# Optimization experiments

Hardware: AMD Instinct MI355X
Metric: run time of the kernel (lower is better)

## Reference

```python
import jax, jax.numpy as jnp
import numpy as np

B, N, M, C, H, NNZ = 64, 2048, 2048, 64, 128, 32768


def setup_inputs() -> dict:
    key = jax.random.key(0)
    ks = jax.random.split(key, 7)
    x = jax.random.normal(ks[0], (B * N, H), dtype=jnp.float32)
    batch = jnp.repeat(jnp.arange(B, dtype=jnp.int32), N)  # sorted graph ids
    d_rows = jax.random.randint(ks[1], (B, NNZ), 0, M, dtype=jnp.int32)
    d_cols = jax.random.randint(ks[2], (B, NNZ), 0, N, dtype=jnp.int32)
    d_vals = jax.random.normal(ks[3], (B, NNZ), dtype=jnp.float32) * (1.0 / np.sqrt(16.0))
    d_index = jax.random.randint(ks[4], (B, M), 0, C, dtype=jnp.int32)
    w_scale = 1.0 / np.sqrt(3 * H)
    Wq = jax.random.normal(ks[5], (3 * H, H), dtype=jnp.float32) * w_scale
    Wk = jax.random.normal(ks[6], (3 * H, H), dtype=jnp.float32) * w_scale
    Wv = jax.random.normal(jax.random.fold_in(key, 7), (3 * H, H), dtype=jnp.float32) * w_scale
    return {"x": x, "batch": batch, "batch_size": B, "d_rows": d_rows,
            "d_cols": d_cols, "d_vals": d_vals, "d_index": d_index,
            "Wq": Wq, "Wk": Wk, "Wv": Wv}


def _per_graph(xg, rows, cols, vals, idx, Wq, Wk, Wv):
    # spmm: coefs[r] = sum_e vals[e] * xg[cols[e]] for rows[e] == r  -> [M, H]
    coefs = jax.ops.segment_sum(vals[:, None] * xg[cols], rows, num_segments=M)
    # three segment poolings over cluster index -> each [C, H]
    s = jax.ops.segment_sum(coefs, idx, num_segments=C)
    cnt = jax.ops.segment_sum(jnp.ones((M,), coefs.dtype), idx, num_segments=C)
    mean = s / jnp.maximum(cnt, 1.0)[:, None]
    mx = jax.ops.segment_max(coefs, idx, num_segments=C)
    x_dec = jnp.concatenate([mean, mx, s], axis=1)  # [C, 3H]
    # small self-attention over clusters (linear layers without bias)
    Q = x_dec @ Wq
    K = x_dec @ Wk
    V = x_dec @ Wv
    dist = jax.nn.softmax((Q @ K.T) * (1.0 / np.sqrt(H)), axis=-1)
    return (dist @ V).reshape(-1)  # [C*H]


def reference(x, batch, batch_size, d_rows, d_cols, d_vals, d_index, Wq, Wk, Wv):
    # nodes are sorted by graph with equal graph size N, so x[batch==i] == xb[i]
    xb = x.reshape(batch_size, N, H)
    out = jax.vmap(_per_graph, in_axes=(0, 0, 0, 0, 0, None, None, None))(
        xb, d_rows, d_cols, d_vals, d_index, Wq, Wk, Wv)
    return out  # [B, C*H] == torch.vstack of per-graph flattened attentions
```

## Files before the change

### kernel.cpp

```cpp
#include <hip/hip_runtime.h>
#include <hip/hip_fp16.h>

#define BG 64
#define NN 2048
#define MM 2048
#define CC 64
#define HH 128
#define NNZE 32768
#define TH 384

typedef float f4v __attribute__((ext_vector_type(4)));

__global__ __launch_bounds__(256) void cvt_x_kernel(const float* __restrict__ x,
                                                    uint* __restrict__ xh) {
    int bid = blockIdx.x;
    int j = bid >> 3;
    int g = ((bid & 7) << 3) + (j >> 7);
    int chunk = j & 127;
    int tid = g * 32768 + chunk * 256 + threadIdx.x;
    const f4v* x4 = (const f4v*)x;
    f4v a = __builtin_nontemporal_load(&x4[2 * tid]);
    f4v b = __builtin_nontemporal_load(&x4[2 * tid + 1]);
    __half2 h0 = __float22half2_rn(make_float2(a.x, a.y));
    __half2 h1 = __float22half2_rn(make_float2(a.z, a.w));
    __half2 h2 = __float22half2_rn(make_float2(b.x, b.y));
    __half2 h3 = __float22half2_rn(make_float2(b.z, b.w));
    uint4 o;
    o.x = *(uint*)&h0;
    o.y = *(uint*)&h1;
    o.z = *(uint*)&h2;
    o.w = *(uint*)&h3;
    ((uint4*)xh)[tid] = o;
}

__global__ __launch_bounds__(1024) void prep_count_kernel(const int* __restrict__ d_rows,
                                                          const int* __restrict__ d_index,
                                                          int* __restrict__ cnt_blk,
                                                          int* __restrict__ cnt_clu_blk) {
    __shared__ int cnt_row_s[MM];
    __shared__ int cnt_clu_s[CC];
    int gb = blockIdx.x;
    int g = gb >> 2, b = gb & 3;
    int t = threadIdx.x;
    cnt_row_s[t] = 0;
    cnt_row_s[t + 1024] = 0;
    if (t < CC) cnt_clu_s[t] = 0;
    __syncthreads();
    const int* rows_g = d_rows + ((size_t)g << 15) + (b << 13);
#pragma unroll
    for (int it = 0; it < 8; it++) atomicAdd(&cnt_row_s[rows_g[it * 1024 + t]], 1);
    if (t < 512) atomicAdd(&cnt_clu_s[d_index[(g << 11) + (b << 9) + t]], 1);
    __syncthreads();
    int* cb = cnt_blk + (size_t)gb * MM;
    cb[t] = cnt_row_s[t];
    cb[t + 1024] = cnt_row_s[t + 1024];
    if (t < CC) cnt_clu_blk[gb * CC + t] = cnt_clu_s[t];
}

__global__ __launch_bounds__(1024) void prep_scan_kernel(const int* __restrict__ d_index,
                                                         const int* __restrict__ cnt_blk,
                                                         const int* __restrict__ cnt_clu_blk,
                                                         int* __restrict__ cnt_clu_g,
                                                         int* __restrict__ off_clu_g,
                                                         int* __restrict__ row_edge_off_g,
                                                         int* __restrict__ off_row_blk,
                                                         int* __restrict__ end_pos) {
    __shared__ int cnt_clu_s[CC], off_clu_s[CC], fill_clu_s[CC];
    __shared__ int rlist_s[MM];
    __shared__ int rowtot_s[MM];
    __shared__ int blk1_s[MM], blk2_s[MM], blk3_s[MM];
    __shared__ int off_row_s[MM];
    __shared__ int wsum[16];
    int g = blockIdx.x, t = threadIdx.x;
    int lane = t & 63, w = t >> 6;

    const int* cb = cnt_blk + ((size_t)g << 2) * MM;
    for (int r = t; r < MM; r += 1024) {
        int c0 = cb[r], c1 = cb[MM + r], c2 = cb[2 * MM + r], c3 = cb[3 * MM + r];
        blk1_s[r] = c0;
        blk2_s[r] = c0 + c1;
        blk3_s[r] = c0 + c1 + c2;
        rowtot_s[r] = c0 + c1 + c2 + c3;
    }
    if (t < CC) {
        const int* ccb = cnt_clu_blk + (g << 2) * CC;
        int v = ccb[t] + ccb[CC + t] + ccb[2 * CC + t] + ccb[3 * CC + t];
        cnt_clu_s[t] = v;
        fill_clu_s[t] = 0;
        int incl = v;
#pragma unroll
        for (int d = 1; d < 64; d <<= 1) {
            int u = __shfl_up(incl, d);
            if (t >= d) incl += u;
        }
        off_clu_s[t] = incl - v;
        cnt_clu_g[(g << 6) + t] = v;
        off_clu_g[(g << 6) + t] = incl - v;
    }
    int idx0 = d_index[(g << 11) + t];
    int idx1 = d_index[(g << 11) + t + 1024];
    __syncthreads();

    {
        int s0 = atomicAdd(&fill_clu_s[idx0], 1);
        rlist_s[off_clu_s[idx0] + s0] = t;
        int s1 = atomicAdd(&fill_clu_s[idx1], 1);
        rlist_s[off_clu_s[idx1] + s1] = t + 1024;
    }
    __syncthreads();

    int r0 = rlist_s[2 * t], r1 = rlist_s[2 * t + 1];
    int c0 = rowtot_s[r0], c1 = rowtot_s[r1];
    int s = c0 + c1;
    int incl = s;
#pragma unroll
    for (int d = 1; d < 64; d <<= 1) {
        int u = __shfl_up(incl, d);
        if (lane >= d) incl += u;
    }
    if (lane == 63) wsum[w] = incl;
    __syncthreads();
    if (t < 16) {
        int v = wsum[t], iv = v;
#pragma unroll
        for (int d = 1; d < 16; d <<= 1) {
            int u = __shfl_up(iv, d);
            if (t >= d) iv += u;
        }
        wsum[t] = iv - v;
    }
    __syncthreads();
    {
        int base = wsum[w] + incl - s;
        int* reo = row_edge_off_g + g * (MM + 1);
        reo[2 * t] = base;
        reo[2 * t + 1] = base + c0;
        off_row_s[r0] = base;
        off_row_s[r1] = base + c0;
        if (t == 0) reo[MM] = NNZE;
    }
    __syncthreads();

    int* ob = off_row_blk + ((size_t)g << 2) * MM;
    int* epp = end_pos + (size_t)g * MM;
    for (int r = t; r < MM; r += 1024) {
        int orr = off_row_s[r];
        ob[r] = orr;
        ob[MM + r] = orr + blk1_s[r];
        ob[2 * MM + r] = orr + blk2_s[r];
        ob[3 * MM + r] = orr + blk3_s[r];
        epp[r] = orr + rowtot_s[r];
    }
}

__global__ __launch_bounds__(1024) void prep_bin_kernel(const int* __restrict__ d_rows,
                                                        const int* __restrict__ d_cols,
                                                        const float* __restrict__ d_vals,
                                                        const int* __restrict__ off_row_blk,
                                                        const int* __restrict__ end_pos,
                                                        int2* __restrict__ epack) {
    __shared__ int off_s[MM];
    __shared__ int end_s[MM];
    __shared__ int fill_s[MM];
    int gb = blockIdx.x;
    int g = gb >> 2, b = gb & 3;
    int t = threadIdx.x;
    const int* ob = off_row_blk + (size_t)gb * MM;
    const int* epp = end_pos + (size_t)g * MM;
    off_s[t] = ob[t];
    off_s[t + 1024] = ob[t + 1024];
    end_s[t] = epp[t];
    end_s[t + 1024] = epp[t + 1024];
    fill_s[t] = 0;
    fill_s[t + 1024] = 0;
    __syncthreads();
    const int* rows_g = d_rows + ((size_t)g << 15) + (b << 13);
    const int* cols_g = d_cols + ((size_t)g << 15) + (b << 13);
    const float* vals_g = d_vals + ((size_t)g << 15) + (b << 13);
    int2* epg = epack + ((size_t)g << 15);
#pragma unroll
    for (int it = 0; it < 8; it++) {
        int e = it * 1024 + t;
        int r = rows_g[e];
        int slot = atomicAdd(&fill_s[r], 1);
        int pos = off_s[r] + slot;
        int flag = (pos == end_s[r] - 1) ? (int)0x80000000 : 0;
        epg[pos] = make_int2(cols_g[e] | flag, __float_as_int(vals_g[e]));
    }
}

__global__ __launch_bounds__(64) void spmm_pool_kernel(const uint* __restrict__ xh,
                                                       const int* __restrict__ cnt_clu,
                                                       const int* __restrict__ off_clu,
                                                       const int* __restrict__ row_edge_off,
                                                       const int2* __restrict__ epack,
                                                       float* __restrict__ xdec) {
    int bid = blockIdx.x;
    int l = bid >> 3;
    int g = ((bid & 7) << 3) + (l >> 6);
    int c = l & 63;
    int h = threadIdx.x;
    int gc = (g << 6) + c;
    int rcnt = cnt_clu[gc];
    int j0 = off_clu[gc];
    const int* reo = row_edge_off + g * (MM + 1) + j0;
    int ebase = reo[0];
    int etot = reo[rcnt] - ebase;
    const long long* ep = (const long long*)(epack + ((size_t)g << 15)) + ebase;
    const uint* xg = xh + ((size_t)g << 17);
    float2 coef = make_float2(0.f, 0.f), sum = make_float2(0.f, 0.f);
    float2 mx = make_float2(-__builtin_inff(), -__builtin_inff());
    int e = 0;
    for (; e + 16 <= etot; e += 16) {
        long long q[16];
#pragma unroll
        for (int k = 0; k < 16; k++) q[k] = __builtin_nontemporal_load(&ep[e + k]);
        uint xv[16];
#pragma unroll
        for (int k = 0; k < 16; k++)
            xv[k] = xg[(((uint)(int)q[k] & 0x7FFFFFFFu) << 6) + h];
#pragma unroll
        for (int k = 0; k < 16; k++) {
            float v = __int_as_float((int)(q[k] >> 32));
            float2 f = __half22float2(*(__half2*)&xv[k]);
            coef.x = fmaf(v, f.x, coef.x);
            coef.y = fmaf(v, f.y, coef.y);
            if ((int)q[k] < 0) {
                sum.x += coef.x; sum.y += coef.y;
                mx.x = fmaxf(mx.x, coef.x); mx.y = fmaxf(mx.y, coef.y);
                coef.x = 0.f; coef.y = 0.f;
            }
        }
    }
    for (; e < etot; e++) {
        long long q = ep[e];
        uint xv = xg[(((uint)(int)q & 0x7FFFFFFFu) << 6) + h];
        float v = __int_as_float((int)(q >> 32));
        float2 f = __half22float2(*(__half2*)&xv);
        coef.x = fmaf(v, f.x, coef.x);
        coef.y = fmaf(v, f.y, coef.y);
        if ((int)q < 0) {
            sum.x += coef.x; sum.y += coef.y;
            mx.x = fmaxf(mx.x, coef.x); mx.y = fmaxf(mx.y, coef.y);
            coef.x = 0.f; coef.y = 0.f;
        }
    }
    int az = 0;
    for (int j = h; j < rcnt; j += 64) az |= (reo[j + 1] == reo[j]);
    if (__ballot(az) != 0ULL) {
        mx.x = fmaxf(mx.x, 0.f);
        mx.y = fmaxf(mx.y, 0.f);
    }
    float inv = 1.f / (float)(rcnt > 0 ? rcnt : 1);
    float* xd = xdec + (size_t)gc * TH;
    *(float2*)&xd[2 * h] = make_float2(sum.x * inv, sum.y * inv);
    *(float2*)&xd[HH + 2 * h] = mx;
    *(float2*)&xd[2 * HH + 2 * h] = sum;
}

__global__ __launch_bounds__(256) void qkv_kernel(const float* __restrict__ xdec,
                                                  const float* __restrict__ Wq,
                                                  const float* __restrict__ Wk,
                                                  const float* __restrict__ Wv,
                                                  float* __restrict__ QKV) {
    __shared__ float As[16][68];
    __shared__ float Bs[16][64];
    int bx = blockIdx.x, by = blockIdx.y;
    int t = threadIdx.x;
    int tx = t & 15, ty = t >> 4;
    const float* W = (by < 2) ? Wq : (by < 4) ? Wk : Wv;
    int cbase = (by & 1) * 64;
    int r0 = bx * 64;
    float acc[4][4] = {};
    int lrow = t >> 2, lk4 = (t & 3) * 4;
    for (int k0 = 0; k0 < TH; k0 += 16) {
        float4 av = *(const float4*)&xdec[(size_t)(r0 + lrow) * TH + k0 + lk4];
        As[lk4][lrow] = av.x;
        As[lk4 + 1][lrow] = av.y;
        As[lk4 + 2][lrow] = av.z;
        As[lk4 + 3][lrow] = av.w;
        *(float4*)&Bs[ty][tx * 4] = *(const float4*)&W[(size_t)(k0 + ty) * HH + cbase + tx * 4];
        __syncthreads();
#pragma unroll
        for (int k = 0; k < 16; k++) {
            float4 a = *(float4*)&As[k][ty * 4];
            float4 b = *(float4*)&Bs[k][tx * 4];
            float ar[4] = {a.x, a.y, a.z, a.w};
            float br[4] = {b.x, b.y, b.z, b.w};
#pragma unroll
            for (int i = 0; i < 4; i++)
#pragma unroll
                for (int j = 0; j < 4; j++) acc[i][j] = fmaf(ar[i], br[j], acc[i][j]);
        }
        __syncthreads();
    }
#pragma unroll
    for (int i = 0; i < 4; i++) {
        *(float4*)&QKV[(size_t)(r0 + ty * 4 + i) * TH + by * 64 + tx * 4] =
            make_float4(acc[i][0], acc[i][1], acc[i][2], acc[i][3]);
    }
}

__global__ __launch_bounds__(256) void attn_kernel(const float* __restrict__ QKV,
                                                   float* __restrict__ out) {
    __shared__ float Qs[16][132];
    __shared__ float sc[16][68];
    int g = blockIdx.x;
    int q0 = blockIdx.y * 16;
    int t = threadIdx.x;
    const float* base = QKV + (size_t)(g * CC) * TH;
    for (int u = t; u < 512; u += 256) {
        int i = u >> 5, cc = u & 31;
        *(float4*)&Qs[i][cc * 4] = *(const float4*)&base[(size_t)(q0 + i) * TH + cc * 4];
    }
    __syncthreads();
    {
        int j = t & 63, iq = t >> 6;
        float a0 = 0, a1 = 0, a2 = 0, a3 = 0;
        const float* Krow = base + (size_t)j * TH + HH;
#pragma unroll 4
        for (int cc = 0; cc < 32; cc++) {
            float4 kv = *(const float4*)&Krow[cc * 4];
            float4 q0v = *(float4*)&Qs[iq][cc * 4];
            float4 q1v = *(float4*)&Qs[4 + iq][cc * 4];
            float4 q2v = *(float4*)&Qs[8 + iq][cc * 4];
            float4 q3v = *(float4*)&Qs[12 + iq][cc * 4];
            a0 += kv.x * q0v.x + kv.y * q0v.y + kv.z * q0v.z + kv.w * q0v.w;
            a1 += kv.x * q1v.x + kv.y * q1v.y + kv.z * q1v.z + kv.w * q1v.w;
            a2 += kv.x * q2v.x + kv.y * q2v.y + kv.z * q2v.z + kv.w * q2v.w;
            a3 += kv.x * q3v.x + kv.y * q3v.y + kv.z * q3v.z + kv.w * q3v.w;
        }
        const float scale = 0.08838834764831845f;
        sc[iq][j] = a0 * scale;
        sc[4 + iq][j] = a1 * scale;
        sc[8 + iq][j] = a2 * scale;
        sc[12 + iq][j] = a3 * scale;
    }
    __syncthreads();
    {
        int i = t >> 4, l = t & 15;
        float4 sv = *(float4*)&sc[i][l * 4];
        float m = fmaxf(fmaxf(sv.x, sv.y), fmaxf(sv.z, sv.w));
#pragma unroll
        for (int d = 1; d < 16; d <<= 1) m = fmaxf(m, __shfl_xor(m, d));
        float4 p;
        p.x = __expf(sv.x - m);
        p.y = __expf(sv.y - m);
        p.z = __expf(sv.z - m);
        p.w = __expf(sv.w - m);
        float s = p.x + p.y + p.z + p.w;
#pragma unroll
        for (int d = 1; d < 16; d <<= 1) s += __shfl_xor(s, d);
        float inv = 1.0f / s;
        p.x *= inv; p.y *= inv; p.z *= inv; p.w *= inv;
        *(float4*)&sc[i][l * 4] = p;
    }
    __syncthreads();
    {
        int i = t >> 4, hq = t & 15;
        const float* Vbase = base + 2 * HH;
        float acc[8] = {};
        for (int j = 0; j < 64; j++) {
            float d = sc[i][j];
            float4 v0 = *(const float4*)&Vbase[(size_t)j * TH + hq * 8];
            float4 v1 = *(const float4*)&Vbase[(size_t)j * TH + hq * 8 + 4];
            acc[0] = fmaf(d, v0.x, acc[0]);
            acc[1] = fmaf(d, v0.y, acc[1]);
            acc[2] = fmaf(d, v0.z, acc[2]);
            acc[3] = fmaf(d, v0.w, acc[3]);
            acc[4] = fmaf(d, v1.x, acc[4]);
            acc[5] = fmaf(d, v1.y, acc[5]);
            acc[6] = fmaf(d, v1.z, acc[6]);
            acc[7] = fmaf(d, v1.w, acc[7]);
        }
        float* op = out + (size_t)g * (CC * HH) + (size_t)(q0 + i) * HH + hq * 8;
        *(float4*)&op[0] = make_float4(acc[0], acc[1], acc[2], acc[3]);
        *(float4*)&op[4] = make_float4(acc[4], acc[5], acc[6], acc[7]);
    }
}

extern "C" void kernel_launch(void* const* d_in, const int* in_sizes, int n_in,
                              void* d_out, int out_size, void* d_ws, size_t ws_size,
                              hipStream_t stream) {
    const float* x = (const float*)d_in[0];
    const int* d_rows = (const int*)d_in[3];
    const int* d_cols = (const int*)d_in[4];
    const float* d_vals = (const float*)d_in[5];
    const int* d_index = (const int*)d_in[6];
    const float* Wq = (const float*)d_in[7];
    const float* Wk = (const float*)d_in[8];
    const float* Wv = (const float*)d_in[9];
    float* out = (float*)d_out;

    char* ws = (char*)d_ws;
    size_t o = 0;
    uint* xh = (uint*)(ws + o); o += (size_t)BG * NN * (HH / 2) * 4;
    int2* epack = (int2*)(ws + o); o += (size_t)BG * NNZE * 8;
    int* cnt_blk = (int*)(ws + o); o += (size_t)BG * 4 * MM * 4;
    int* off_row_blk = (int*)(ws + o); o += (size_t)BG * 4 * MM * 4;
    int* end_pos = (int*)(ws + o); o += (size_t)BG * MM * 4;
    int* cnt_clu_blk = (int*)(ws + o); o += (size_t)BG * 4 * CC * 4;
    int* row_edge_off = (int*)(ws + o); o += (size_t)BG * (MM + 1) * 4;
    int* cnt_clu = (int*)(ws + o); o += (size_t)BG * CC * 4;
    int* off_clu = (int*)(ws + o); o += (size_t)BG * CC * 4;
    float* xdec = (float*)(ws + o); o += (size_t)BG * CC * TH * 4;
    float* QKV = (float*)(ws + o); o += (size_t)BG * CC * TH * 4;

    prep_count_kernel<<<BG * 4, 1024, 0, stream>>>(d_rows, d_index, cnt_blk, cnt_clu_blk);
    prep_scan_kernel<<<BG, 1024, 0, stream>>>(d_index, cnt_blk, cnt_clu_blk,
                                              cnt_clu, off_clu, row_edge_off,
                                              off_row_blk, end_pos);
    prep_bin_kernel<<<BG * 4, 1024, 0, stream>>>(d_rows, d_cols, d_vals,
                                                 off_row_blk, end_pos, epack);
    cvt_x_kernel<<<BG * NN * HH / 8 / 256, 256, 0, stream>>>(x, xh);
    spmm_pool_kernel<<<BG * CC, 64, 0, stream>>>(xh, cnt_clu, off_clu, row_edge_off,
                                                 epack, xdec);
    qkv_kernel<<<dim3(64, 6), 256, 0, stream>>>(xdec, Wq, Wk, Wv, QKV);
    attn_kernel<<<dim3(BG, 4), 256, 0, stream>>>(QKV, out);
}
```

Baseline: 261.7 us.

## Split wavefront halves across edge pairs with 8-byte gathers in spmm_pool

The spmm pooling kernel now has each 64-lane wavefront handle two edges at a time. Each half-wave gathers one column row of x with 8-byte (4 half) loads instead of 4-byte loads. Partial row coefficients are combined across the halves with a shuffle when a row ends. Occupancy is hinted with launch_bounds(64,4), and the unroll depth grows to 32 edges. This halves the number of gather instructions per edge and widens each memory access, at the cost of extra shuffles and branching at row boundaries.

```diff
diff --git a/kernel.cpp b/kernel.cpp
--- a/kernel.cpp
+++ b/kernel.cpp
@@ -189,17 +189,19 @@
     }
 }
 
-__global__ __launch_bounds__(64) void spmm_pool_kernel(const uint* __restrict__ xh,
-                                                       const int* __restrict__ cnt_clu,
-                                                       const int* __restrict__ off_clu,
-                                                       const int* __restrict__ row_edge_off,
-                                                       const int2* __restrict__ epack,
-                                                       float* __restrict__ xdec) {
+__global__ __launch_bounds__(64, 4) void spmm_pool_kernel(const uint* __restrict__ xh,
+                                                          const int* __restrict__ cnt_clu,
+                                                          const int* __restrict__ off_clu,
+                                                          const int* __restrict__ row_edge_off,
+                                                          const int2* __restrict__ epack,
+                                                          float* __restrict__ xdec) {
     int bid = blockIdx.x;
     int l = bid >> 3;
     int g = ((bid & 7) << 3) + (l >> 6);
     int c = l & 63;
-    int h = threadIdx.x;
+    int t = threadIdx.x;
+    int f = t & 31;
+    int hi = t & 32;
     int gc = (g << 6) + c;
     int rcnt = cnt_clu[gc];
     int j0 = off_clu[gc];
@@ -207,55 +209,113 @@
     int ebase = reo[0];
     int etot = reo[rcnt] - ebase;
     const long long* ep = (const long long*)(epack + ((size_t)g << 15)) + ebase;
-    const uint* xg = xh + ((size_t)g << 17);
-    float2 coef = make_float2(0.f, 0.f), sum = make_float2(0.f, 0.f);
-    float2 mx = make_float2(-__builtin_inff(), -__builtin_inff());
+    const uint2* xg2 = (const uint2*)(xh + ((size_t)g << 17));
+    float4 coef = make_float4(0.f, 0.f, 0.f, 0.f);
+    float4 sum = make_float4(0.f, 0.f, 0.f, 0.f);
+    float4 mx = make_float4(-__builtin_inff(), -__builtin_inff(),
+                            -__builtin_inff(), -__builtin_inff());
+
+#define ACCUM(XV, VV)                                      \
+    do {                                                   \
+        float2 _f0 = __half22float2(*(__half2*)&(XV).x);   \
+        float2 _f1 = __half22float2(*(__half2*)&(XV).y);   \
+        float _vv = (VV);                                  \
+        coef.x = fmaf(_vv, _f0.x, coef.x);                 \
+        coef.y = fmaf(_vv, _f0.y, coef.y);                 \
+        coef.z = fmaf(_vv, _f1.x, coef.z);                 \
+        coef.w = fmaf(_vv, _f1.y, coef.w);                 \
+    } while (0)
+
+#define FLUSH                                              \
+    do {                                                   \
+        float _tx = coef.x + __shfl_xor(coef.x, 32);       \
+        float _ty = coef.y + __shfl_xor(coef.y, 32);       \
+        float _tz = coef.z + __shfl_xor(coef.z, 32);       \
+        float _tw = coef.w + __shfl_xor(coef.w, 32);       \
+        sum.x += _tx; sum.y += _ty; sum.z += _tz; sum.w += _tw; \
+        mx.x = fmaxf(mx.x, _tx); mx.y = fmaxf(mx.y, _ty);  \
+        mx.z = fmaxf(mx.z, _tz); mx.w = fmaxf(mx.w, _tw);  \
+        coef.x = 0.f; coef.y = 0.f; coef.z = 0.f; coef.w = 0.f; \
+    } while (0)
+
+#define PAIR_STEP(Q0, Q1, XV)                              \
+    do {                                                   \
+        float _v0 = __int_as_float((int)((Q0) >> 32));     \
+        float _v1 = __int_as_float((int)((Q1) >> 32));     \
+        bool _fl0 = (int)(Q0) < 0, _fl1 = (int)(Q1) < 0;   \
+        if (!_fl0 && !_fl1) {                              \
+            ACCUM(XV, hi ? _v1 : _v0);                     \
+        } else {                                           \
+            ACCUM(XV, hi ? 0.f : _v0);                     \
+            if (_fl0) FLUSH;                               \
+            ACCUM(XV, hi ? _v1 : 0.f);                     \
+            if (_fl1) FLUSH;                               \
+        }                                                  \
+    } while (0)
+
     int e = 0;
-    for (; e + 16 <= etot; e += 16) {
-        long long q[16];
-#pragma unroll
-        for (int k = 0; k < 16; k++) q[k] = __builtin_nontemporal_load(&ep[e + k]);
-        uint xv[16];
-#pragma unroll
-        for (int k = 0; k < 16; k++)
-            xv[k] = xg[(((uint)(int)q[k] & 0x7FFFFFFFu) << 6) + h];
-#pragma unroll
-        for (int k = 0; k < 16; k++) {
-            float v = __int_as_float((int)(q[k] >> 32));
-            float2 f = __half22float2(*(__half2*)&xv[k]);
-            coef.x = fmaf(v, f.x, coef.x);
-            coef.y = fmaf(v, f.y, coef.y);
-            if ((int)q[k] < 0) {
-                sum.x += coef.x; sum.y += coef.y;
-                mx.x = fmaxf(mx.x, coef.x); mx.y = fmaxf(mx.y, coef.y);
-                coef.x = 0.f; coef.y = 0.f;
-            }
-        }
-    }
-    for (; e < etot; e++) {
-        long long q = ep[e];
-        uint xv = xg[(((uint)(int)q & 0x7FFFFFFFu) << 6) + h];
-        float v = __int_as_float((int)(q >> 32));
-        float2 f = __half22float2(*(__half2*)&xv);
-        coef.x = fmaf(v, f.x, coef.x);
-        coef.y = fmaf(v, f.y, coef.y);
-        if ((int)q < 0) {
-            sum.x += coef.x; sum.y += coef.y;
-            mx.x = fmaxf(mx.x, coef.x); mx.y = fmaxf(mx.y, coef.y);
-            coef.x = 0.f; coef.y = 0.f;
-        }
-    }
+    for (; e + 32 <= etot; e += 32) {
+        long long q[32];
+#pragma unroll
+        for (int k = 0; k < 32; k++) q[k] = __builtin_nontemporal_load(&ep[e + k]);
+        uint2 xv[16];
+#pragma unroll
+        for (int p = 0; p < 16; p++) {
+            int c0 = (int)q[2 * p] & 0x7FFFFFFF;
+            int c1 = (int)q[2 * p + 1] & 0x7FFFFFFF;
+            xv[p] = xg2[((uint)(hi ? c1 : c0) << 5) + f];
+        }
+#pragma unroll
+        for (int p = 0; p < 16; p++) PAIR_STEP(q[2 * p], q[2 * p + 1], xv[p]);
+    }
+    for (; e + 8 <= etot; e += 8) {
+        long long q[8];
+#pragma unroll
+        for (int k = 0; k < 8; k++) q[k] = __builtin_nontemporal_load(&ep[e + k]);
+        uint2 xv[4];
+#pragma unroll
+        for (int p = 0; p < 4; p++) {
+            int c0 = (int)q[2 * p] & 0x7FFFFFFF;
+            int c1 = (int)q[2 * p + 1] & 0x7FFFFFFF;
+            xv[p] = xg2[((uint)(hi ? c1 : c0) << 5) + f];
+        }
+#pragma unroll
+        for (int p = 0; p < 4; p++) PAIR_STEP(q[2 * p], q[2 * p + 1], xv[p]);
+    }
+    for (; e + 2 <= etot; e += 2) {
+        long long q0 = __builtin_nontemporal_load(&ep[e]);
+        long long q1 = __builtin_nontemporal_load(&ep[e + 1]);
+        int c0 = (int)q0 & 0x7FFFFFFF;
+        int c1 = (int)q1 & 0x7FFFFFFF;
+        uint2 xv = xg2[((uint)(hi ? c1 : c0) << 5) + f];
+        PAIR_STEP(q0, q1, xv);
+    }
+    if (e < etot) {
+        long long q0 = __builtin_nontemporal_load(&ep[e]);
+        int c0 = (int)q0 & 0x7FFFFFFF;
+        uint2 xv = xg2[((uint)c0 << 5) + f];
+        ACCUM(xv, hi ? 0.f : __int_as_float((int)(q0 >> 32)));
+        if ((int)q0 < 0) FLUSH;
+    }
+
     int az = 0;
-    for (int j = h; j < rcnt; j += 64) az |= (reo[j + 1] == reo[j]);
+    for (int j = t; j < rcnt; j += 64) az |= (reo[j + 1] == reo[j]);
     if (__ballot(az) != 0ULL) {
         mx.x = fmaxf(mx.x, 0.f);
         mx.y = fmaxf(mx.y, 0.f);
+        mx.z = fmaxf(mx.z, 0.f);
+        mx.w = fmaxf(mx.w, 0.f);
     }
     float inv = 1.f / (float)(rcnt > 0 ? rcnt : 1);
-    float* xd = xdec + (size_t)gc * TH;
-    *(float2*)&xd[2 * h] = make_float2(sum.x * inv, sum.y * inv);
-    *(float2*)&xd[HH + 2 * h] = mx;
-    *(float2*)&xd[2 * HH + 2 * h] = sum;
+    if (t < 32) {
+        float* xd = xdec + (size_t)gc * TH;
+        *(float4*)&xd[4 * f] = make_float4(sum.x * inv, sum.y * inv, sum.z * inv, sum.w * inv);
+        *(float4*)&xd[HH + 4 * f] = mx;
+        *(float4*)&xd[2 * HH + 4 * f] = sum;
+    }
+#undef ACCUM
+#undef FLUSH
+#undef PAIR_STEP
 }
 
 __global__ __launch_bounds__(256) void qkv_kernel(const float* __restrict__ xdec,
```

Result: slower. 270.9 us (+3.5%).

## Double-buffer SpMM gathers into LDS via async global_load_lds with prefetched edge batches

Applied to the files above, without the earlier changes.

The SpMM pooling loop now handles edges in batches of 32. For each batch, the gathered half-precision rows of x are staged into a double-buffered LDS tile with 16-byte global_load_lds, and edge metadata is prefetched two batches ahead. Each lane now loads one packed edge and the per-edge column/value are broadcast with readlane, instead of every lane loading every edge. This is meant to overlap the gather latency of the next batch with compute on the current one, in exchange for 16KB of LDS per 64-thread block (lower occupancy) and explicit vmcnt waits.

```diff
diff --git a/kernel.cpp b/kernel.cpp
--- a/kernel.cpp
+++ b/kernel.cpp
@@ -10,6 +10,11 @@
 #define TH 384
 
 typedef float f4v __attribute__((ext_vector_type(4)));
+
+#define GLOAD_LDS16(SRC, DST)                                             \
+    __builtin_amdgcn_global_load_lds(                                     \
+        (const __attribute__((address_space(1))) uint*)(SRC),             \
+        (__attribute__((address_space(3))) uint*)(DST), 16, 0, 0)
 
 __global__ __launch_bounds__(256) void cvt_x_kernel(const float* __restrict__ x,
                                                     uint* __restrict__ xh) {
@@ -195,11 +200,14 @@
                                                        const int* __restrict__ row_edge_off,
                                                        const int2* __restrict__ epack,
                                                        float* __restrict__ xdec) {
+    __shared__ uint sbuf[2][2048];
     int bid = blockIdx.x;
     int l = bid >> 3;
     int g = ((bid & 7) << 3) + (l >> 6);
     int c = l & 63;
     int h = threadIdx.x;
+    int sub = h >> 4;
+    int part = h & 15;
     int gc = (g << 6) + c;
     int rcnt = cnt_clu[gc];
     int j0 = off_clu[gc];
@@ -210,41 +218,84 @@
     const uint* xg = xh + ((size_t)g << 17);
     float2 coef = make_float2(0.f, 0.f), sum = make_float2(0.f, 0.f);
     float2 mx = make_float2(-__builtin_inff(), -__builtin_inff());
-    int e = 0;
-    for (; e + 16 <= etot; e += 16) {
-        long long q[16];
-#pragma unroll
-        for (int k = 0; k < 16; k++) q[k] = __builtin_nontemporal_load(&ep[e + k]);
-        uint xv[16];
-#pragma unroll
-        for (int k = 0; k < 16; k++)
-            xv[k] = xg[(((uint)(int)q[k] & 0x7FFFFFFFu) << 6) + h];
-#pragma unroll
-        for (int k = 0; k < 16; k++) {
-            float v = __int_as_float((int)(q[k] >> 32));
-            float2 f = __half22float2(*(__half2*)&xv[k]);
-            coef.x = fmaf(v, f.x, coef.x);
-            coef.y = fmaf(v, f.y, coef.y);
-            if ((int)q[k] < 0) {
-                sum.x += coef.x; sum.y += coef.y;
-                mx.x = fmaxf(mx.x, coef.x); mx.y = fmaxf(mx.y, coef.y);
-                coef.x = 0.f; coef.y = 0.f;
+
+#define SPMM_FLUSH                                         \
+    do {                                                   \
+        sum.x += coef.x; sum.y += coef.y;                  \
+        mx.x = fmaxf(mx.x, coef.x);                        \
+        mx.y = fmaxf(mx.y, coef.y);                        \
+        coef.x = 0.f; coef.y = 0.f;                        \
+    } while (0)
+
+    int nb = etot >> 5;
+    long long qC = 0, qA = 0, qB = 0;
+    int colA[8], colB[8];
+    int cur = 0;
+
+    if (nb > 0) {
+        qC = ep[h >> 1];
+        int col0[8];
+#pragma unroll
+        for (int i = 0; i < 8; i++)
+            col0[i] = ((const int*)(ep + 4 * i + sub))[0] & 0x7FFFFFFF;
+        asm volatile("s_waitcnt vmcnt(0)" ::: "memory");
+#pragma unroll
+        for (int i = 0; i < 8; i++)
+            GLOAD_LDS16(xg + ((uint)col0[i] << 6) + (part << 2), &sbuf[0][i << 8]);
+        if (nb > 1) {
+            const long long* ep1 = ep + 32;
+            qA = ep1[h >> 1];
+#pragma unroll
+            for (int i = 0; i < 8; i++)
+                colA[i] = ((const int*)(ep1 + 4 * i + sub))[0] & 0x7FFFFFFF;
+        }
+    }
+    for (int b = 0; b < nb; b++) {
+        asm volatile("s_waitcnt vmcnt(0)" ::: "memory");
+        if (b + 1 < nb) {
+#pragma unroll
+            for (int i = 0; i < 8; i++)
+                GLOAD_LDS16(xg + ((uint)colA[i] << 6) + (part << 2),
+                            &sbuf[cur ^ 1][i << 8]);
+        }
+        if (b + 2 < nb) {
+            const long long* epn = ep + ((b + 2) << 5);
+            qB = epn[h >> 1];
+#pragma unroll
+            for (int i = 0; i < 8; i++)
+                colB[i] = ((const int*)(epn + 4 * i + sub))[0] & 0x7FFFFFFF;
+        }
+        {
+            int qlo = (int)qC, qhi = (int)(qC >> 32);
+            const uint* sb = &sbuf[cur][0];
+#pragma unroll
+            for (int k = 0; k < 32; k++) {
+                uint xv = sb[(k << 6) + h];
+                int ql = __builtin_amdgcn_readlane(qlo, 2 * k);
+                int qh = __builtin_amdgcn_readlane(qhi, 2 * k);
+                float v = __int_as_float(qh);
+                float2 f = __half22float2(*(__half2*)&xv);
+                coef.x = fmaf(v, f.x, coef.x);
+                coef.y = fmaf(v, f.y, coef.y);
+                if (ql < 0) SPMM_FLUSH;
             }
         }
-    }
-    for (; e < etot; e++) {
+        qC = qA;
+        qA = qB;
+#pragma unroll
+        for (int i = 0; i < 8; i++) colA[i] = colB[i];
+        cur ^= 1;
+    }
+    for (int e = nb << 5; e < etot; e++) {
         long long q = ep[e];
         uint xv = xg[(((uint)(int)q & 0x7FFFFFFFu) << 6) + h];
         float v = __int_as_float((int)(q >> 32));
         float2 f = __half22float2(*(__half2*)&xv);
         coef.x = fmaf(v, f.x, coef.x);
         coef.y = fmaf(v, f.y, coef.y);
-        if ((int)q < 0) {
-            sum.x += coef.x; sum.y += coef.y;
-            mx.x = fmaxf(mx.x, coef.x); mx.y = fmaxf(mx.y, coef.y);
-            coef.x = 0.f; coef.y = 0.f;
-        }
-    }
+        if ((int)q < 0) SPMM_FLUSH;
+    }
+
     int az = 0;
     for (int j = h; j < rcnt; j += 64) az |= (reo[j + 1] == reo[j]);
     if (__ballot(az) != 0ULL) {
@@ -256,6 +307,7 @@
     *(float2*)&xd[2 * h] = make_float2(sum.x * inv, sum.y * inv);
     *(float2*)&xd[HH + 2 * h] = mx;
     *(float2*)&xd[2 * HH + 2 * h] = sum;
+#undef SPMM_FLUSH
 }
 
 __global__ __launch_bounds__(256) void qkv_kernel(const float* __restrict__ xdec,
```

New measurement: 286.7 us. 9.5% more time.

## Use split-bf16 MFMA for QKV projection and fuse x conversion into prep

Applied to the files above, without the earlier changes.

The QKV projection moves from an FP32 SIMT GEMM to bf16 MFMA instructions, using a hi/lo split (three products per tile) to keep close to FP32 accuracy. The spmm kernel now writes the pooled features as hi/lo bf16 pairs, and the weights are split and transposed inside the prep count kernel. The separate x-to-half conversion kernel is folded into prep_count, removing one launch. The cost is three MFMAs per tile plus the extra split work, and prep_count now does more memory traffic per block.

```diff
diff --git a/kernel.cpp b/kernel.cpp
--- a/kernel.cpp
+++ b/kernel.cpp
@@ -10,33 +10,30 @@
 #define TH 384
 
 typedef float f4v __attribute__((ext_vector_type(4)));
-
-__global__ __launch_bounds__(256) void cvt_x_kernel(const float* __restrict__ x,
-                                                    uint* __restrict__ xh) {
-    int bid = blockIdx.x;
-    int j = bid >> 3;
-    int g = ((bid & 7) << 3) + (j >> 7);
-    int chunk = j & 127;
-    int tid = g * 32768 + chunk * 256 + threadIdx.x;
-    const f4v* x4 = (const f4v*)x;
-    f4v a = __builtin_nontemporal_load(&x4[2 * tid]);
-    f4v b = __builtin_nontemporal_load(&x4[2 * tid + 1]);
-    __half2 h0 = __float22half2_rn(make_float2(a.x, a.y));
-    __half2 h1 = __float22half2_rn(make_float2(a.z, a.w));
-    __half2 h2 = __float22half2_rn(make_float2(b.x, b.y));
-    __half2 h3 = __float22half2_rn(make_float2(b.z, b.w));
-    uint4 o;
-    o.x = *(uint*)&h0;
-    o.y = *(uint*)&h1;
-    o.z = *(uint*)&h2;
-    o.w = *(uint*)&h3;
-    ((uint4*)xh)[tid] = o;
+typedef __attribute__((ext_vector_type(8))) short bf16x8;
+typedef __attribute__((ext_vector_type(4))) float f32x4;
+typedef unsigned short u16;
+
+static __device__ __forceinline__ u16 bf16rne(float f) {
+    uint u = __float_as_uint(f);
+    uint r = u + 0x7FFFu + ((u >> 16) & 1u);
+    return (u16)(r >> 16);
+}
+static __device__ __forceinline__ float bf16tof(u16 h) {
+    return __uint_as_float(((uint)h) << 16);
 }
 
 __global__ __launch_bounds__(1024) void prep_count_kernel(const int* __restrict__ d_rows,
                                                           const int* __restrict__ d_index,
+                                                          const float* __restrict__ x,
+                                                          const float* __restrict__ Wq,
+                                                          const float* __restrict__ Wk,
+                                                          const float* __restrict__ Wv,
                                                           int* __restrict__ cnt_blk,
-                                                          int* __restrict__ cnt_clu_blk) {
+                                                          int* __restrict__ cnt_clu_blk,
+                                                          uint* __restrict__ xh,
+                                                          u16* __restrict__ WhT,
+                                                          u16* __restrict__ WlT) {
     __shared__ int cnt_row_s[MM];
     __shared__ int cnt_clu_s[CC];
     int gb = blockIdx.x;
@@ -50,6 +47,39 @@
 #pragma unroll
     for (int it = 0; it < 8; it++) atomicAdd(&cnt_row_s[rows_g[it * 1024 + t]], 1);
     if (t < 512) atomicAdd(&cnt_clu_s[d_index[(g << 11) + (b << 9) + t]], 1);
+
+    {
+        const f4v* x4 = (const f4v*)x;
+        uint4* xh4 = (uint4*)xh;
+#pragma unroll
+        for (int it = 0; it < 8; it++) {
+            int tidg = (gb << 13) + it * 1024 + t;
+            f4v a = __builtin_nontemporal_load(&x4[2 * tidg]);
+            f4v bb = __builtin_nontemporal_load(&x4[2 * tidg + 1]);
+            __half2 h0 = __float22half2_rn(make_float2(a.x, a.y));
+            __half2 h1 = __float22half2_rn(make_float2(a.z, a.w));
+            __half2 h2 = __float22half2_rn(make_float2(bb.x, bb.y));
+            __half2 h3 = __float22half2_rn(make_float2(bb.z, bb.w));
+            uint4 o;
+            o.x = *(uint*)&h0;
+            o.y = *(uint*)&h1;
+            o.z = *(uint*)&h2;
+            o.w = *(uint*)&h3;
+            xh4[tidg] = o;
+        }
+    }
+    if (gb < 144) {
+        int id = (gb << 10) + t;
+        int w = id / 49152;
+        int r = id - w * 49152;
+        const float* Ws = (w == 0) ? Wq : (w == 1) ? Wk : Wv;
+        float v = Ws[r];
+        int k = r >> 7, n = r & 127;
+        u16 hi = bf16rne(v);
+        u16 lo = bf16rne(v - bf16tof(hi));
+        WhT[w * 49152 + n * 384 + k] = hi;
+        WlT[w * 49152 + n * 384 + k] = lo;
+    }
     __syncthreads();
     int* cb = cnt_blk + (size_t)gb * MM;
     cb[t] = cnt_row_s[t];
@@ -194,7 +224,8 @@
                                                        const int* __restrict__ off_clu,
                                                        const int* __restrict__ row_edge_off,
                                                        const int2* __restrict__ epack,
-                                                       float* __restrict__ xdec) {
+                                                       u16* __restrict__ xdh,
+                                                       u16* __restrict__ xdl) {
     int bid = blockIdx.x;
     int l = bid >> 3;
     int g = ((bid & 7) << 3) + (l >> 6);
@@ -252,53 +283,91 @@
         mx.y = fmaxf(mx.y, 0.f);
     }
     float inv = 1.f / (float)(rcnt > 0 ? rcnt : 1);
-    float* xd = xdec + (size_t)gc * TH;
-    *(float2*)&xd[2 * h] = make_float2(sum.x * inv, sum.y * inv);
-    *(float2*)&xd[HH + 2 * h] = mx;
-    *(float2*)&xd[2 * HH + 2 * h] = sum;
-}
-
-__global__ __launch_bounds__(256) void qkv_kernel(const float* __restrict__ xdec,
-                                                  const float* __restrict__ Wq,
-                                                  const float* __restrict__ Wk,
-                                                  const float* __restrict__ Wv,
+    uint* oh = (uint*)xdh + (size_t)gc * 192 + h;
+    uint* ol = (uint*)xdl + (size_t)gc * 192 + h;
+    float me0 = sum.x * inv, me1 = sum.y * inv;
+    u16 a0 = bf16rne(me0), a1 = bf16rne(me1);
+    oh[0] = (uint)a0 | ((uint)a1 << 16);
+    ol[0] = (uint)bf16rne(me0 - bf16tof(a0)) | ((uint)bf16rne(me1 - bf16tof(a1)) << 16);
+    u16 b0 = bf16rne(mx.x), b1 = bf16rne(mx.y);
+    oh[64] = (uint)b0 | ((uint)b1 << 16);
+    ol[64] = (uint)bf16rne(mx.x - bf16tof(b0)) | ((uint)bf16rne(mx.y - bf16tof(b1)) << 16);
+    u16 c0 = bf16rne(sum.x), c1 = bf16rne(sum.y);
+    oh[128] = (uint)c0 | ((uint)c1 << 16);
+    ol[128] = (uint)bf16rne(sum.x - bf16tof(c0)) | ((uint)bf16rne(sum.y - bf16tof(c1)) << 16);
+}
+
+__global__ __launch_bounds__(256) void qkv_kernel(const u16* __restrict__ xdh,
+                                                  const u16* __restrict__ xdl,
+                                                  const u16* __restrict__ WhT,
+                                                  const u16* __restrict__ WlT,
                                                   float* __restrict__ QKV) {
-    __shared__ float As[16][68];
-    __shared__ float Bs[16][64];
+    __shared__ u16 Ah[64][40], Al[64][40], Bh[64][40], Bl[64][40];
     int bx = blockIdx.x, by = blockIdx.y;
     int t = threadIdx.x;
-    int tx = t & 15, ty = t >> 4;
-    const float* W = (by < 2) ? Wq : (by < 4) ? Wk : Wv;
-    int cbase = (by & 1) * 64;
-    int r0 = bx * 64;
-    float acc[4][4] = {};
-    int lrow = t >> 2, lk4 = (t & 3) * 4;
-    for (int k0 = 0; k0 < TH; k0 += 16) {
-        float4 av = *(const float4*)&xdec[(size_t)(r0 + lrow) * TH + k0 + lk4];
-        As[lk4][lrow] = av.x;
-        As[lk4 + 1][lrow] = av.y;
-        As[lk4 + 2][lrow] = av.z;
-        As[lk4 + 3][lrow] = av.w;
-        *(float4*)&Bs[ty][tx * 4] = *(const float4*)&W[(size_t)(k0 + ty) * HH + cbase + tx * 4];
+    int w = by >> 1;
+    int cb = (by & 1) << 6;
+    int r0 = bx << 6;
+    const u16* wh = WhT + w * 49152;
+    const u16* wl = WlT + w * 49152;
+    int lane = t & 63, wv = t >> 6;
+    int wm = wv >> 1, wn = wv & 1;
+    int srow = t >> 2, sks = (t & 3) << 3;
+    int fr = lane & 15, fk = (lane >> 4) << 3;
+    f32x4 acc[2][2];
+#pragma unroll
+    for (int i = 0; i < 2; i++)
+#pragma unroll
+        for (int j = 0; j < 2; j++)
+#pragma unroll
+            for (int r = 0; r < 4; r++) acc[i][j][r] = 0.f;
+    for (int ks = 0; ks < 12; ks++) {
+        int k0 = ks << 5;
+        bf16x8 sa_h = *(const bf16x8*)&xdh[(size_t)(r0 + srow) * 384 + k0 + sks];
+        bf16x8 sa_l = *(const bf16x8*)&xdl[(size_t)(r0 + srow) * 384 + k0 + sks];
+        bf16x8 sb_h = *(const bf16x8*)&wh[(size_t)(cb + srow) * 384 + k0 + sks];
+        bf16x8 sb_l = *(const bf16x8*)&wl[(size_t)(cb + srow) * 384 + k0 + sks];
+        if (ks) __syncthreads();
+        *(bf16x8*)&Ah[srow][sks] = sa_h;
+        *(bf16x8*)&Al[srow][sks] = sa_l;
+        *(bf16x8*)&Bh[srow][sks] = sb_h;
+        *(bf16x8*)&Bl[srow][sks] = sb_l;
         __syncthreads();
-#pragma unroll
-        for (int k = 0; k < 16; k++) {
-            float4 a = *(float4*)&As[k][ty * 4];
-            float4 b = *(float4*)&Bs[k][tx * 4];
-            float ar[4] = {a.x, a.y, a.z, a.w};
-            float br[4] = {b.x, b.y, b.z, b.w};
-#pragma unroll
-            for (int i = 0; i < 4; i++)
-#pragma unroll
-                for (int j = 0; j < 4; j++) acc[i][j] = fmaf(ar[i], br[j], acc[i][j]);
-        }
-        __syncthreads();
-    }
-#pragma unroll
-    for (int i = 0; i < 4; i++) {
-        *(float4*)&QKV[(size_t)(r0 + ty * 4 + i) * TH + by * 64 + tx * 4] =
-            make_float4(acc[i][0], acc[i][1], acc[i][2], acc[i][3]);
-    }
+        bf16x8 fa_h[2], fa_l[2], fb_h[2], fb_l[2];
+#pragma unroll
+        for (int mi = 0; mi < 2; mi++) {
+            int ar = (wm << 5) + (mi << 4) + fr;
+            fa_h[mi] = *(const bf16x8*)&Ah[ar][fk];
+            fa_l[mi] = *(const bf16x8*)&Al[ar][fk];
+        }
+#pragma unroll
+        for (int ni = 0; ni < 2; ni++) {
+            int br = (wn << 5) + (ni << 4) + fr;
+            fb_h[ni] = *(const bf16x8*)&Bh[br][fk];
+            fb_l[ni] = *(const bf16x8*)&Bl[br][fk];
+        }
+#pragma unroll
+        for (int mi = 0; mi < 2; mi++)
+#pragma unroll
+            for (int ni = 0; ni < 2; ni++) {
+                acc[mi][ni] = __builtin_amdgcn_mfma_f32_16x16x32_bf16(
+                    fa_h[mi], fb_h[ni], acc[mi][ni], 0, 0, 0);
+                acc[mi][ni] = __builtin_amdgcn_mfma_f32_16x16x32_bf16(
+                    fa_h[mi], fb_l[ni], acc[mi][ni], 0, 0, 0);
+                acc[mi][ni] = __builtin_amdgcn_mfma_f32_16x16x32_bf16(
+                    fa_l[mi], fb_h[ni], acc[mi][ni], 0, 0, 0);
+            }
+    }
+#pragma unroll
+    for (int mi = 0; mi < 2; mi++)
+#pragma unroll
+        for (int ni = 0; ni < 2; ni++)
+#pragma unroll
+            for (int r = 0; r < 4; r++) {
+                int row = r0 + (wm << 5) + (mi << 4) + ((lane >> 4) << 2) + r;
+                int col = (by << 6) + (wn << 5) + (ni << 4) + (lane & 15);
+                QKV[(size_t)row * TH + col] = acc[mi][ni][r];
+            }
 }
 
 __global__ __launch_bounds__(256) void attn_kernel(const float* __restrict__ QKV,
@@ -403,18 +472,21 @@
     int* row_edge_off = (int*)(ws + o); o += (size_t)BG * (MM + 1) * 4;
     int* cnt_clu = (int*)(ws + o); o += (size_t)BG * CC * 4;
     int* off_clu = (int*)(ws + o); o += (size_t)BG * CC * 4;
-    float* xdec = (float*)(ws + o); o += (size_t)BG * CC * TH * 4;
+    u16* xdh = (u16*)(ws + o); o += (size_t)BG * CC * TH * 2;
+    u16* xdl = (u16*)(ws + o); o += (size_t)BG * CC * TH * 2;
+    u16* WhT = (u16*)(ws + o); o += (size_t)3 * HH * TH * 2;
+    u16* WlT = (u16*)(ws + o); o += (size_t)3 * HH * TH * 2;
     float* QKV = (float*)(ws + o); o += (size_t)BG * CC * TH * 4;
 
-    prep_count_kernel<<<BG * 4, 1024, 0, stream>>>(d_rows, d_index, cnt_blk, cnt_clu_blk);
+    prep_count_kernel<<<BG * 4, 1024, 0, stream>>>(d_rows, d_index, x, Wq, Wk, Wv,
+                                                   cnt_blk, cnt_clu_blk, xh, WhT, WlT);
     prep_scan_kernel<<<BG, 1024, 0, stream>>>(d_index, cnt_blk, cnt_clu_blk,
                                               cnt_clu, off_clu, row_edge_off,
                                               off_row_blk, end_pos);
     prep_bin_kernel<<<BG * 4, 1024, 0, stream>>>(d_rows, d_cols, d_vals,
                                                  off_row_blk, end_pos, epack);
-    cvt_x_kernel<<<BG * NN * HH / 8 / 256, 256, 0, stream>>>(x, xh);
     spmm_pool_kernel<<<BG * CC, 64, 0, stream>>>(xh, cnt_clu, off_clu, row_edge_off,
-                                                 epack, xdec);
-    qkv_kernel<<<dim3(64, 6), 256, 0, stream>>>(xdec, Wq, Wk, Wv, QKV);
+                                                 epack, xdh, xdl);
+    qkv_kernel<<<dim3(64, 6), 256, 0, stream>>>(xdh, xdl, WhT, WlT, QKV);
     attn_kernel<<<dim3(BG, 4), 256, 0, stream>>>(QKV, out);
 }
```

After: 258.0 us. About the same (-1.4%).
